# Optimization experiments

Measured on AMD Instinct MI355X. Metric: run time of the kernel, lower is better.

## Reference

```python
import jax, jax.numpy as jnp
import numpy as np

NUM_USERS = 500000
NUM_ITEMS = 300000
NUM_NODES = NUM_USERS + NUM_ITEMS
NUM_EDGES = 1250000
DIM = 64
N_LAYERS = 3


def setup_inputs() -> dict:
    key = jax.random.key(0)
    k1, k2, k3, k4 = jax.random.split(key, 4)
    user_emb = 0.1 * jax.random.normal(k1, (NUM_USERS, DIM), dtype=jnp.float32)
    item_emb = 0.1 * jax.random.normal(k2, (NUM_ITEMS, DIM), dtype=jnp.float32)
    src = jax.random.randint(k3, (NUM_EDGES,), 0, NUM_NODES, dtype=jnp.int32)
    dst = jax.random.randint(k4, (NUM_EDGES,), 0, NUM_NODES, dtype=jnp.int32)
    return {"user_emb": user_emb, "item_emb": item_emb, "src": src, "dst": dst}


def reference(user_emb, item_emb, src, dst):
    n = NUM_NODES
    ones = jnp.ones_like(src, dtype=jnp.float32)
    # DGL GraphConv norm='both': D_out^{-1/2} on source side, D_in^{-1/2} on dest side,
    # degrees clamped to min 1 (allow_zero_in_degree=True).
    deg_out = jnp.clip(jax.ops.segment_sum(ones, src, num_segments=n), 1.0)
    deg_in = jnp.clip(jax.ops.segment_sum(ones, dst, num_segments=n), 1.0)
    src_norm = deg_out ** -0.5  # [N]
    dst_norm = deg_in ** -0.5   # [N]

    def conv(h):  # [N, D] -> [N, D]
        h = h * src_norm[:, None]
        msg = h[src]                                        # [E, D] gather
        agg = jax.ops.segment_sum(msg, dst, num_segments=n)  # [N, D] scatter-add
        return agg * dst_norm[:, None]

    h = jnp.concatenate([user_emb, item_emb], axis=0)  # [N, D]
    acc = h
    for _ in range(N_LAYERS):
        h = conv(h)
        acc = acc + h
    light_out = acc / (N_LAYERS + 1)  # mean over stacked layer embeddings
    users = light_out[:NUM_USERS]
    items = light_out[NUM_USERS:]
    return users, items
```

## Files before the change

### kernel.cpp

```cpp
#include <hip/hip_runtime.h>


static constexpr int NU = 500000;
static constexpr int NI = 300000;
static constexpr int NN = NU + NI;
static constexpr int NE = 1250000;
static constexpr int DIM = 64;
static constexpr int CHUNK = 1024;
static constexpr int NCHUNK = (NN + CHUNK - 1) / CHUNK;

__global__ void hist_kernel(const int* __restrict__ src, const int* __restrict__ dst,
                            int* __restrict__ cout, int* __restrict__ cin) {
    int e = blockIdx.x * blockDim.x + threadIdx.x;
    if (e < NE) {
        atomicAdd(&cout[src[e]], 1);
        atomicAdd(&cin[dst[e]], 1);
    }
}

__global__ void norm_kernel(const int* __restrict__ cout, const int* __restrict__ cin,
                            float* __restrict__ sn, float* __restrict__ dn,
                            float* __restrict__ comb) {
    int i = blockIdx.x * blockDim.x + threadIdx.x;
    if (i < NN) {
        float a = rsqrtf(fmaxf((float)cout[i], 1.0f));
        float b = rsqrtf(fmaxf((float)cin[i], 1.0f));
        sn[i] = a; dn[i] = b; comb[i] = a * b;
    }
}

__global__ void scan_chunks(const int* __restrict__ cnt, int* __restrict__ chunkSum) {
    int b = blockIdx.x, t = threadIdx.x;
    int idx = b * CHUNK + t * 4;
    int s = 0;
    #pragma unroll
    for (int k = 0; k < 4; ++k) { int j = idx + k; if (j < NN) s += cnt[j]; }
    for (int off = 32; off; off >>= 1) s += __shfl_down(s, off);
    __shared__ int ws[4];
    if ((t & 63) == 0) ws[t >> 6] = s;
    __syncthreads();
    if (t == 0) chunkSum[b] = ws[0] + ws[1] + ws[2] + ws[3];
}

__global__ void scan_offsets(int* __restrict__ chunkSum) {
    int t = threadIdx.x;
    const int G = 4;
    int loc[G]; int s = 0;
    #pragma unroll
    for (int k = 0; k < G; ++k) { int j = t * G + k; int v = (j < NCHUNK) ? chunkSum[j] : 0; loc[k] = s; s += v; }
    int ss = s;
    for (int off = 1; off < 64; off <<= 1) { int n = __shfl_up(ss, off); if ((t & 63) >= off) ss += n; }
    __shared__ int wtot[4];
    if ((t & 63) == 63) wtot[t >> 6] = ss;
    __syncthreads();
    int woff = 0;
    for (int w = 0; w < (t >> 6); ++w) woff += wtot[w];
    int excl = woff + ss - s;
    #pragma unroll
    for (int k = 0; k < G; ++k) { int j = t * G + k; if (j < NCHUNK) chunkSum[j] = excl + loc[k]; }
}

__global__ void scan_fill(const int* __restrict__ cnt, const int* __restrict__ chunkOff,
                          int* __restrict__ cursor) {
    int b = blockIdx.x, t = threadIdx.x;
    int idx = b * CHUNK + t * 4;
    int v[4]; int s = 0;
    #pragma unroll
    for (int k = 0; k < 4; ++k) { int j = idx + k; int c = (j < NN) ? cnt[j] : 0; v[k] = s; s += c; }
    int ss = s;
    for (int off = 1; off < 64; off <<= 1) { int n = __shfl_up(ss, off); if ((t & 63) >= off) ss += n; }
    __shared__ int wtot[4];
    if ((t & 63) == 63) wtot[t >> 6] = ss;
    __syncthreads();
    int woff = 0;
    for (int w = 0; w < (t >> 6); ++w) woff += wtot[w];
    int excl = woff + (ss - s) + chunkOff[b];
    #pragma unroll
    for (int k = 0; k < 4; ++k) { int j = idx + k; if (j < NN) cursor[j] = excl + v[k]; }
}

__global__ void scatter_kernel(const int* __restrict__ src, const int* __restrict__ dst,
                               int* __restrict__ cursor, int* __restrict__ eSrc) {
    int e = blockIdx.x * blockDim.x + threadIdx.x;
    if (e < NE) {
        int p = atomicAdd(&cursor[dst[e]], 1);
        eSrc[p] = src[e];
    }
}

template <int LAYER>
__global__ void layer_kernel(const float* __restrict__ ue, const float* __restrict__ ie,
                             const float* __restrict__ g,
                             const int* __restrict__ cursor, const int* __restrict__ eSrc,
                             const float* __restrict__ sn, const float* __restrict__ dn,
                             const float* __restrict__ comb,
                             const float* __restrict__ g1,
                             float* __restrict__ outbuf) {
    int t = blockIdx.x * blockDim.x + threadIdx.x;
    int v = t >> 6;
    if (v >= NN) return;
    int d = t & 63;
    int end = cursor[v];
    int start = (v == 0) ? 0 : cursor[v - 1];
    float acc = 0.0f;
    for (int i = start; i < end; ++i) {
        int s = eSrc[i];
        float w, hv;
        if (LAYER == 1) {
            w = sn[s];
            hv = (s < NU) ? ue[(size_t)s * DIM + d] : ie[(size_t)(s - NU) * DIM + d];
        } else {
            w = comb[s];
            hv = g[(size_t)s * DIM + d];
        }
        acc = fmaf(w, hv, acc);
    }
    if (LAYER < 3) {
        outbuf[(size_t)v * DIM + d] = acc;
    } else {
        float h0 = (v < NU) ? ue[(size_t)v * DIM + d] : ie[(size_t)(v - NU) * DIM + d];
        float gs = g1[(size_t)v * DIM + d] + g[(size_t)v * DIM + d] + acc;
        outbuf[(size_t)v * DIM + d] = 0.25f * (h0 + gs * dn[v]);
    }
}

extern "C" void kernel_launch(void* const* d_in, const int* in_sizes, int n_in,
                              void* d_out, int out_size, void* d_ws, size_t ws_size,
                              hipStream_t stream) {
    const float* ue = (const float*)d_in[0];
    const float* ie = (const float*)d_in[1];
    const int* src = (const int*)d_in[2];
    const int* dst = (const int*)d_in[3];
    float* out = (float*)d_out;

    int* cout = (int*)d_ws;
    int* cin = cout + NN;
    int* cursor = cin + NN;
    int* chunkSum = cursor + NN;
    int* eSrc = chunkSum + 1024;
    float* sn = (float*)(eSrc + NE);
    float* dn = sn + NN;
    float* comb = dn + NN;
    float* g2 = comb + NN;

    const int EB = (NE + 255) / 256;
    const int NB = (NN + 255) / 256;
    const int LB = (NN * 64 + 255) / 256;

    hipMemsetAsync(cout, 0, (size_t)2 * NN * sizeof(int), stream);
    hist_kernel<<<EB, 256, 0, stream>>>(src, dst, cout, cin);
    norm_kernel<<<NB, 256, 0, stream>>>(cout, cin, sn, dn, comb);
    scan_chunks<<<NCHUNK, 256, 0, stream>>>(cin, chunkSum);
    scan_offsets<<<1, 256, 0, stream>>>(chunkSum);
    scan_fill<<<NCHUNK, 256, 0, stream>>>(cin, chunkSum, cursor);
    scatter_kernel<<<EB, 256, 0, stream>>>(src, dst, cursor, eSrc);

    layer_kernel<1><<<LB, 256, 0, stream>>>(ue, ie, nullptr, cursor, eSrc, sn, dn, comb, nullptr, out);
    layer_kernel<2><<<LB, 256, 0, stream>>>(ue, ie, out, cursor, eSrc, sn, dn, comb, nullptr, g2);
    layer_kernel<3><<<LB, 256, 0, stream>>>(ue, ie, g2, cursor, eSrc, sn, dn, comb, out, out);
}
```

Before: 1.402 ms.

## Store pre-scaled layer messages in fp16 to halve gather traffic

Adds a prep kernel that pre-multiplies the input embeddings by the source norm and stores them as fp16. Each layer now writes the next message pre-scaled by the combined norm, so the gather loop reads one fp16 value and does a plain add, with no per-edge weight load. The final layer rebuilds the unscaled sums by multiplying by the square root of the out-degree. The random gather reads half the bytes, in exchange for fp16 rounding error in the intermediate embeddings and an extra full pass to build the fp16 copy.

```diff
diff --git a/kernel.cpp b/kernel.cpp
--- a/kernel.cpp
+++ b/kernel.cpp
@@ -1,4 +1,5 @@
 #include <hip/hip_runtime.h>
+#include <hip/hip_fp16.h>
 
 
 static constexpr int NU = 500000;
@@ -20,12 +21,13 @@
 
 __global__ void norm_kernel(const int* __restrict__ cout, const int* __restrict__ cin,
                             float* __restrict__ sn, float* __restrict__ dn,
-                            float* __restrict__ comb) {
+                            float* __restrict__ comb, float* __restrict__ rn) {
     int i = blockIdx.x * blockDim.x + threadIdx.x;
     if (i < NN) {
-        float a = rsqrtf(fmaxf((float)cout[i], 1.0f));
+        float fo = fmaxf((float)cout[i], 1.0f);
+        float a = rsqrtf(fo);
         float b = rsqrtf(fmaxf((float)cin[i], 1.0f));
-        sn[i] = a; dn[i] = b; comb[i] = a * b;
+        sn[i] = a; dn[i] = b; comb[i] = a * b; rn[i] = sqrtf(fo);
     }
 }
 
@@ -88,39 +90,46 @@
     }
 }
 
+__global__ void prep_kernel(const float* __restrict__ ue, const float* __restrict__ ie,
+                            const float* __restrict__ sn, __half* __restrict__ m0) {
+    int t = blockIdx.x * blockDim.x + threadIdx.x;
+    if (t >= NN * 16) return;
+    int n = t >> 4; int q = t & 15;
+    float w = sn[n];
+    float4 h = (n < NU) ? reinterpret_cast<const float4*>(ue)[(size_t)n * 16 + q]
+                        : reinterpret_cast<const float4*>(ie)[(size_t)(n - NU) * 16 + q];
+    __half2 a = __floats2half2_rn(w * h.x, w * h.y);
+    __half2 b = __floats2half2_rn(w * h.z, w * h.w);
+    reinterpret_cast<__half2*>(m0)[(size_t)t * 2]     = a;
+    reinterpret_cast<__half2*>(m0)[(size_t)t * 2 + 1] = b;
+}
+
 template <int LAYER>
-__global__ void layer_kernel(const float* __restrict__ ue, const float* __restrict__ ie,
-                             const float* __restrict__ g,
-                             const int* __restrict__ cursor, const int* __restrict__ eSrc,
-                             const float* __restrict__ sn, const float* __restrict__ dn,
-                             const float* __restrict__ comb,
-                             const float* __restrict__ g1,
-                             float* __restrict__ outbuf) {
+__global__ void layer_kernel(const __half* __restrict__ min_,
+                             const int* __restrict__ rowend, const int* __restrict__ eSrc,
+                             const float* __restrict__ comb, __half* __restrict__ mout,
+                             const __half* __restrict__ m1, const __half* __restrict__ m2,
+                             const float* __restrict__ rn, const float* __restrict__ dn,
+                             const float* __restrict__ ue, const float* __restrict__ ie,
+                             float* __restrict__ out) {
     int t = blockIdx.x * blockDim.x + threadIdx.x;
     int v = t >> 6;
     if (v >= NN) return;
     int d = t & 63;
-    int end = cursor[v];
-    int start = (v == 0) ? 0 : cursor[v - 1];
+    int end = rowend[v];
+    int start = (v == 0) ? 0 : rowend[v - 1];
     float acc = 0.0f;
     for (int i = start; i < end; ++i) {
         int s = eSrc[i];
-        float w, hv;
-        if (LAYER == 1) {
-            w = sn[s];
-            hv = (s < NU) ? ue[(size_t)s * DIM + d] : ie[(size_t)(s - NU) * DIM + d];
-        } else {
-            w = comb[s];
-            hv = g[(size_t)s * DIM + d];
-        }
-        acc = fmaf(w, hv, acc);
+        acc += __half2float(min_[(size_t)s * DIM + d]);
     }
+    size_t idx = (size_t)v * DIM + d;
     if (LAYER < 3) {
-        outbuf[(size_t)v * DIM + d] = acc;
+        mout[idx] = __float2half(comb[v] * acc);
     } else {
-        float h0 = (v < NU) ? ue[(size_t)v * DIM + d] : ie[(size_t)(v - NU) * DIM + d];
-        float gs = g1[(size_t)v * DIM + d] + g[(size_t)v * DIM + d] + acc;
-        outbuf[(size_t)v * DIM + d] = 0.25f * (h0 + gs * dn[v]);
+        float h0 = (v < NU) ? ue[idx] : ie[idx - (size_t)NU * DIM];
+        float ms = __half2float(m1[idx]) + __half2float(m2[idx]);
+        out[idx] = 0.25f * (h0 + ms * rn[v] + dn[v] * acc);
     }
 }
 
@@ -141,21 +150,30 @@
     float* sn = (float*)(eSrc + NE);
     float* dn = sn + NN;
     float* comb = dn + NN;
-    float* g2 = comb + NN;
+    float* rn = comb + NN;
+    __half* m0 = (__half*)(rn + NN);
+    __half* m1 = m0 + (size_t)NN * DIM;
+    __half* m2 = m1 + (size_t)NN * DIM;
 
     const int EB = (NE + 255) / 256;
     const int NB = (NN + 255) / 256;
+    const int PB = (NN * 16 + 255) / 256;
     const int LB = (NN * 64 + 255) / 256;
 
     hipMemsetAsync(cout, 0, (size_t)2 * NN * sizeof(int), stream);
     hist_kernel<<<EB, 256, 0, stream>>>(src, dst, cout, cin);
-    norm_kernel<<<NB, 256, 0, stream>>>(cout, cin, sn, dn, comb);
+    norm_kernel<<<NB, 256, 0, stream>>>(cout, cin, sn, dn, comb, rn);
     scan_chunks<<<NCHUNK, 256, 0, stream>>>(cin, chunkSum);
     scan_offsets<<<1, 256, 0, stream>>>(chunkSum);
     scan_fill<<<NCHUNK, 256, 0, stream>>>(cin, chunkSum, cursor);
     scatter_kernel<<<EB, 256, 0, stream>>>(src, dst, cursor, eSrc);
 
-    layer_kernel<1><<<LB, 256, 0, stream>>>(ue, ie, nullptr, cursor, eSrc, sn, dn, comb, nullptr, out);
-    layer_kernel<2><<<LB, 256, 0, stream>>>(ue, ie, out, cursor, eSrc, sn, dn, comb, nullptr, g2);
-    layer_kernel<3><<<LB, 256, 0, stream>>>(ue, ie, g2, cursor, eSrc, sn, dn, comb, out, out);
+    prep_kernel<<<PB, 256, 0, stream>>>(ue, ie, sn, m0);
+
+    layer_kernel<1><<<LB, 256, 0, stream>>>(m0, cursor, eSrc, comb, m1,
+                                            nullptr, nullptr, rn, dn, ue, ie, out);
+    layer_kernel<2><<<LB, 256, 0, stream>>>(m1, cursor, eSrc, comb, m2,
+                                            nullptr, nullptr, rn, dn, ue, ie, out);
+    layer_kernel<3><<<LB, 256, 0, stream>>>(m2, cursor, eSrc, comb, nullptr,
+                                            m1, m2, rn, dn, ue, ie, out);
 }
```

After: 1.319 ms. 1.06x faster.
